# Kernel tuning notes

Measured on AMD Instinct MI355X. Metric: run time of the kernel, lower is better.

## Reference

```python
import jax, jax.numpy as jnp
import numpy as np

N_QUBITS = 2
N_PARAMS = 3 * N_QUBITS - 1  # = 5
B = 65536
C64 = jnp.complex64


def bkron(A, Bm):
    # batched Kronecker product: A [b,m,n], Bm [b,p,q] -> [b,m*p,n*q]
    b, m, n = A.shape
    _, p, q = Bm.shape
    return jnp.einsum('bij,bkl->bikjl', A, Bm).reshape(b, m * p, n * q)


def rx(theta):
    # exp(-0.5j*theta*X) = cos(t/2) I - i sin(t/2) X ; theta [b] real -> [b,2,2] complex
    c = jnp.cos(theta / 2).astype(C64)
    s = (-1j * jnp.sin(theta / 2)).astype(C64)
    return jnp.stack([jnp.stack([c, s], -1), jnp.stack([s, c], -1)], -2)


def ry(theta):
    # exp(-0.5j*theta*Y) = [[cos,-sin],[sin,cos]]
    c = jnp.cos(theta / 2).astype(C64)
    s = jnp.sin(theta / 2).astype(C64)
    return jnp.stack([jnp.stack([c, -s], -1), jnp.stack([s, c], -1)], -2)


def crx(theta):
    # kron(I2, |0><0|) + kron(Rx(theta), |1><1|)  (control on second qubit, as in source)
    b = theta.shape[0]
    P0 = jnp.array([[1, 0], [0, 0]], C64)
    P1 = jnp.array([[0, 0], [0, 1]], C64)
    I2 = jnp.eye(2, dtype=C64)
    term0 = jnp.kron(I2, P0)  # [4,4]
    term1 = bkron(rx(theta), jnp.broadcast_to(P1, (b, 2, 2)))
    return term0[None] + term1


def quantum_state(p):
    # p [b, >=5]; faithful to source: col 0 unused, Rx(p1) applied on both qubits
    first = bkron(rx(p[:, 1]), rx(p[:, 1]))          # recursiveRx, counter=1 base case
    second = bkron(ry(p[:, 2]), ry(p[:, 3]))         # recursiveRy, counter=3 base case
    rot = first @ second
    return rot @ crx(p[:, 4])                        # single CRx layer (N_Qubits=2)


def mlp(h, W1, b1, W2, b2, W3, b3, W4, b4):
    h = jax.nn.relu(h @ W1.T + b1)
    h = jax.nn.relu(h @ W2.T + b2)
    h = jax.nn.relu(h @ W3.T + b3)
    return h @ W4.T + b4


def mH(M):
    return jnp.conj(jnp.swapaxes(M, -1, -2))


def setup_inputs() -> dict:
    key = jax.random.key(0)
    ks = jax.random.split(key, 9)
    dims = [(200, 300), (100, 200), (50, 100), (N_PARAMS * 2, 50)]
    inp = {'x': jax.random.normal(ks[0], (B, 600), dtype=jnp.float32)}
    for i, (o, ii) in enumerate(dims):
        inp[f'W{i+1}'] = jax.random.normal(ks[1 + 2 * i], (o, ii), dtype=jnp.float32) * (1.0 / np.sqrt(ii))
        inp[f'b{i+1}'] = jax.random.normal(ks[2 + 2 * i], (o,), dtype=jnp.float32) * 0.01
    return inp


def reference(x, W1, b1, W2, b2, W3, b3, W4, b4):
    l1 = mlp(x[:, 0:300], W1, b1, W2, b2, W3, b3, W4, b4)   # [B, 10]
    l2 = mlp(x[:, 300:600], W1, b1, W2, b2, W3, b3, W4, b4)  # [B, 10]
    ket = jnp.zeros((4, 1), C64).at[0, 0].set(1.0)
    bra = jnp.zeros((1, 4), C64).at[0, 0].set(1.0)
    U2a = quantum_state(l2[:, :N_PARAMS])
    U2b = quantum_state(l2[:, N_PARAMS:])
    U1a = quantum_state(l1[:, :N_PARAMS])
    U1b = quantum_state(l1[:, N_PARAMS:])
    circuit1 = (bra[None] @ mH(U2a)) @ mH(U2b)   # [B,1,4]
    circuit2 = U1b @ (U1a @ ket[None])           # [B,4,1]
    inner = (circuit1 @ circuit2)[:, 0, 0]       # [B]
    fidelity = jnp.square(jnp.abs(inner))        # [B] real
    return fidelity
```

## Files before the change

kernel.cpp:

```cpp
#include <hip/hip_runtime.h>
#include <hip/hip_bf16.h>
#include <stdint.h>

typedef unsigned short u16;
typedef unsigned int   u32;
typedef __bf16 bf16x8 __attribute__((ext_vector_type(8)));
typedef float  f32x16 __attribute__((ext_vector_type(16)));

__device__ __forceinline__ u16 b2u(__bf16 b){ union U{__bf16 b; u16 u;} v; v.b=b; return v.u; }

__device__ __forceinline__ f32x16 MFMA(bf16x8 a, bf16x8 b, f32x16 c) {
  return __builtin_amdgcn_mfma_f32_32x32x16_bf16(a, b, c, 0, 0, 0);
}

#define OFF_WA  32768
#define OFF_WB  75776
#define LDS_BYTES 118784

constexpr int CH1 = 43008;
constexpr int CH2 = 32768;
constexpr int CH3 = 16384;
constexpr int CH4 = 8192;
constexpr long B1 = 0;
constexpr long B2 = 147L * 2048;
constexpr long B3 = 211L * 2048;
constexpr long B4 = 227L * 2048;

__global__ __launch_bounds__(64) void prep_kernel(
    const float* __restrict__ W1, const float* __restrict__ W2,
    const float* __restrict__ W3, const float* __restrict__ W4,
    u16* __restrict__ wf)
{
  int b = blockIdx.x, lane = threadIdx.x;
  const float* W; int NT, rel, Nv, Kv;
  if (b < 147)      { W = W1; NT = 7; rel = b;       Nv = 200; Kv = 300; }
  else if (b < 211) { W = W2; NT = 4; rel = b - 147; Nv = 100; Kv = 200; }
  else if (b < 227) { W = W3; NT = 2; rel = b - 211; Nv = 50;  Kv = 100; }
  else              { W = W4; NT = 1; rel = b - 227; Nv = 10;  Kv = 50;  }
  int kc = rel / NT, nt = rel % NT;
  int n  = nt*32 + (lane & 31);
  int kb = kc*16 + ((lane >> 5) << 3);
  u16* dst = wf + (size_t)b * 1024;
  #pragma unroll
  for (int j = 0; j < 8; ++j) {
    int k = kb + j;
    float w = (n < Nv && k < Kv) ? W[n*Kv + k] : 0.0f;
    __bf16 h = (__bf16)w;
    __bf16 l = (__bf16)(w - (float)h);
    dst[lane*8 + j]       = b2u(h);
    dst[512 + lane*8 + j] = b2u(l);
  }
}

template<int CHUNK>
__device__ __forceinline__ void stage_load(const char* __restrict__ g, float4* r, int tid) {
  constexpr int NS = (CHUNK + 8191) / 8192;
  #pragma unroll
  for (int it = 0; it < NS; ++it) {
    const int off = tid*16 + it*8192;
    if ((it+1)*8192 <= CHUNK)  r[it] = *(const float4*)(g + off);
    else if (off < CHUNK)      r[it] = *(const float4*)(g + off);
  }
}
template<int CHUNK>
__device__ __forceinline__ void stage_write(char* lds, const float4* r, int tid) {
  constexpr int NS = (CHUNK + 8191) / 8192;
  #pragma unroll
  for (int it = 0; it < NS; ++it) {
    const int off = tid*16 + it*8192;
    if ((it+1)*8192 <= CHUNK)  *(float4*)(lds + off) = r[it];
    else if (off < CHUNK)      *(float4*)(lds + off) = r[it];
  }
}
#define VMCNT0 asm volatile("s_waitcnt vmcnt(0)" ::: "memory")

template<int NTILES>
__device__ __forceinline__ void transition(
    const f32x16* acc, const float* __restrict__ bias, int nvalid,
    bf16x8* hh, bf16x8* hl, char* ms, int lane)
{
  #pragma unroll
  for (int j = 0; j < NTILES; ++j) {
    const int col = j*32 + (lane & 31);
    const float bv = (col < nvalid) ? bias[col] : 0.0f;
    #pragma unroll
    for (int r = 0; r < 16; ++r) {
      const int row = (r & 3) + ((r >> 2) << 3) + (((lane >> 5) & 1) << 2);
      float v = fmaxf(acc[j][r] + bv, 0.0f);
      __bf16 h = (__bf16)v;
      __bf16 l = (__bf16)(v - (float)h);
      const int bo = row*64 + (((lane & 31) << 1) ^ ((row & 3) << 4));
      *(u16*)(ms + bo)        = b2u(h);
      *(u16*)(ms + 2048 + bo) = b2u(l);
    }
    #pragma unroll
    for (int h2 = 0; h2 < 2; ++h2) {
      const int row = lane & 31;
      const int bo = row*64 + ((h2*32 + ((lane >> 5) << 4)) ^ ((row & 3) << 4));
      hh[2*j + h2] = *(const bf16x8*)(ms + bo);
      hl[2*j + h2] = *(const bf16x8*)(ms + 2048 + bo);
    }
  }
}

struct cpx { float r, i; };
__device__ __forceinline__ void ry_pair(float c, float s, cpx& a, cpx& b) {
  cpx na = { c*a.r - s*b.r, c*a.i - s*b.i };
  cpx nb = { s*a.r + c*b.r, s*a.i + c*b.i };
  a = na; b = nb;
}
__device__ __forceinline__ void rx_pair(float c, float s, cpx& a, cpx& b) {
  cpx na = { c*a.r + s*b.i, c*a.i - s*b.r };
  cpx nb = { s*a.i + c*b.r, -s*a.r + c*b.i };
  a = na; b = nb;
}
__device__ void build_state(const float* p, cpx v[4]) {
  float a1 = 0.5f*p[1], a2 = 0.5f*p[2], a3 = 0.5f*p[3];
  float c2 = cosf(a2), s2 = sinf(a2), c3 = cosf(a3), s3 = sinf(a3);
  v[0] = { c2*c3, 0.f }; v[1] = { c2*s3, 0.f };
  v[2] = { s2*c3, 0.f }; v[3] = { s2*s3, 0.f };
  float c1 = cosf(a1), s1 = sinf(a1);
  rx_pair(c1, s1, v[0], v[1]); rx_pair(c1, s1, v[2], v[3]);
  rx_pair(c1, s1, v[0], v[2]); rx_pair(c1, s1, v[1], v[3]);
  float q1 = 0.5f*p[6], q2 = 0.5f*p[7], q3 = 0.5f*p[8], q4 = 0.5f*p[9];
  float c4 = cosf(q4), s4 = sinf(q4);
  rx_pair(c4, s4, v[1], v[3]);
  float cc = cosf(q3), ss = sinf(q3);
  ry_pair(cc, ss, v[0], v[1]); ry_pair(cc, ss, v[2], v[3]);
  cc = cosf(q2); ss = sinf(q2);
  ry_pair(cc, ss, v[0], v[2]); ry_pair(cc, ss, v[1], v[3]);
  cc = cosf(q1); ss = sinf(q1);
  rx_pair(cc, ss, v[0], v[1]); rx_pair(cc, ss, v[2], v[3]);
  rx_pair(cc, ss, v[0], v[2]); rx_pair(cc, ss, v[1], v[3]);
}

__global__ __launch_bounds__(512, 2) void fused_kernel(
    const float* __restrict__ X,
    const float* __restrict__ b1p, const float* __restrict__ b2p,
    const float* __restrict__ b3p, const float* __restrict__ b4p,
    const u16* __restrict__ wf,
    float* __restrict__ out)
{
  __shared__ char lds[LDS_BYTES] __attribute__((aligned(16)));
  const int tid  = threadIdx.x;
  const int lane = tid & 63;
  const int wid  = tid >> 6;
  const long rowbase = (long)blockIdx.x*256 + wid*32;
  char* ms = lds + wid*4096;
  const char* wfc = (const char*)wf;

  float4 s0[6];
  stage_load<CH1>(wfc + B1, s0, tid);

  bf16x8 xf[19];
  {
    const float* xp = X + (rowbase + (lane & 31))*300 + ((lane >> 5) << 3);
    #pragma unroll
    for (int kc = 0; kc < 19; ++kc) {
      float4 f0 = *(const float4*)(xp + kc*16);
      float4 f1;
      if (kc == 18) {
        if (lane >= 32) f1 = make_float4(0.f, 0.f, 0.f, 0.f);
        else            f1 = *(const float4*)(xp + kc*16 + 4);
      } else {
        f1 = *(const float4*)(xp + kc*16 + 4);
      }
      xf[kc][0]=(__bf16)f0.x; xf[kc][1]=(__bf16)f0.y; xf[kc][2]=(__bf16)f0.z; xf[kc][3]=(__bf16)f0.w;
      xf[kc][4]=(__bf16)f1.x; xf[kc][5]=(__bf16)f1.y; xf[kc][6]=(__bf16)f1.z; xf[kc][7]=(__bf16)f1.w;
    }
  }
  VMCNT0;
  stage_write<CH1>(lds + OFF_WA, s0, tid);
  __syncthreads();

  f32x16 acc1[7] = {};
  #pragma unroll
  for (int step = 0; step < 7; ++step) {
    float4 sr[6];
    if (step < 6) stage_load<CH1>(wfc + B1 + (size_t)(step+1)*CH1, sr, tid);
    const char* wb = lds + ((step & 1) ? OFF_WB : OFF_WA);
    #pragma unroll
    for (int kk = 0; kk < 3; ++kk) {
      const int kc = step*3 + kk;
      if (kc < 19) {
        const bf16x8 ah = xf[kc];
        #pragma unroll
        for (int nt = 0; nt < 7; ++nt) {
          const char* bp = wb + (kk*7 + nt)*2048 + lane*16;
          bf16x8 bh = *(const bf16x8*)bp;
          bf16x8 bl = *(const bf16x8*)(bp + 1024);
          acc1[nt] = MFMA(ah, bh, acc1[nt]);
          acc1[nt] = MFMA(ah, bl, acc1[nt]);
        }
      }
    }
    if (step < 6) { VMCNT0; stage_write<CH1>(lds + ((step & 1) ? OFF_WA : OFF_WB), sr, tid); }
    __syncthreads();
  }

  float4 s2[4];
  stage_load<CH2>(wfc + B2, s2, tid);
  bf16x8 h1h[14], h1l[14];
  transition<7>(acc1, b1p, 200, h1h, h1l, ms, lane);
  VMCNT0;
  stage_write<CH2>(lds + OFF_WA, s2, tid);
  __syncthreads();

  f32x16 acc2[4] = {};
  #pragma unroll
  for (int step = 0; step < 4; ++step) {
    float4 sr[4];
    if (step < 3) stage_load<CH2>(wfc + B2 + (size_t)(step+1)*CH2, sr, tid);
    const char* wb = lds + ((step & 1) ? OFF_WB : OFF_WA);
    #pragma unroll
    for (int kk = 0; kk < 4; ++kk) {
      const int kc = step*4 + kk;
      if (kc < 14) {
        #pragma unroll
        for (int nt = 0; nt < 4; ++nt) {
          const char* bp = wb + (kk*4 + nt)*2048 + lane*16;
          bf16x8 bh = *(const bf16x8*)bp;
          bf16x8 bl = *(const bf16x8*)(bp + 1024);
          acc2[nt] = MFMA(h1h[kc], bh, acc2[nt]);
          acc2[nt] = MFMA(h1h[kc], bl, acc2[nt]);
          acc2[nt] = MFMA(h1l[kc], bh, acc2[nt]);
        }
      }
    }
    if (step < 3) { VMCNT0; stage_write<CH2>(lds + ((step & 1) ? OFF_WA : OFF_WB), sr, tid); }
    __syncthreads();
  }

  float4 s3[2];
  stage_load<CH3>(wfc + B3, s3, tid);
  bf16x8 h2h[8], h2l[8];
  transition<4>(acc2, b2p, 100, h2h, h2l, ms, lane);
  VMCNT0;
  stage_write<CH3>(lds + OFF_WA, s3, tid);
  __syncthreads();

  f32x16 acc3[2] = {};
  #pragma unroll
  for (int step = 0; step < 2; ++step) {
    float4 sr[2];
    if (step < 1) stage_load<CH3>(wfc + B3 + (size_t)CH3, sr, tid);
    const char* wb = lds + ((step & 1) ? OFF_WB : OFF_WA);
    #pragma unroll
    for (int kk = 0; kk < 4; ++kk) {
      const int kc = step*4 + kk;
      #pragma unroll
      for (int nt = 0; nt < 2; ++nt) {
        const char* bp = wb + (kk*2 + nt)*2048 + lane*16;
        bf16x8 bh = *(const bf16x8*)bp;
        bf16x8 bl = *(const bf16x8*)(bp + 1024);
        acc3[nt] = MFMA(h2h[kc], bh, acc3[nt]);
        acc3[nt] = MFMA(h2h[kc], bl, acc3[nt]);
        acc3[nt] = MFMA(h2l[kc], bh, acc3[nt]);
      }
    }
    if (step < 1) { VMCNT0; stage_write<CH3>(lds + OFF_WB, sr, tid); }
    __syncthreads();
  }

  float4 s4[1];
  stage_load<CH4>(wfc + B4, s4, tid);
  bf16x8 h3h[4], h3l[4];
  transition<2>(acc3, b3p, 50, h3h, h3l, ms, lane);
  VMCNT0;
  stage_write<CH4>(lds + OFF_WA, s4, tid);
  __syncthreads();

  f32x16 acc4 = {};
  {
    const char* wb = lds + OFF_WA;
    #pragma unroll
    for (int kk = 0; kk < 4; ++kk) {
      const char* bp = wb + kk*2048 + lane*16;
      bf16x8 bh = *(const bf16x8*)bp;
      bf16x8 bl = *(const bf16x8*)(bp + 1024);
      acc4 = MFMA(h3h[kk], bh, acc4);
      acc4 = MFMA(h3h[kk], bl, acc4);
      acc4 = MFMA(h3l[kk], bh, acc4);
    }
  }

  {
    float* sp = (float*)ms;
    #pragma unroll
    for (int r = 0; r < 16; ++r) {
      const int row = (r & 3) + ((r >> 2) << 3) + (((lane >> 5) & 1) << 2);
      const int col = lane & 31;
      sp[row*32 + col] = acc4[r] + ((col < 10) ? b4p[col] : 0.0f);
    }
    if (lane < 16) {
      float p1[10], p2[10];
      #pragma unroll
      for (int j = 0; j < 10; ++j) {
        p1[j] = sp[(2*lane)*32 + j];
        p2[j] = sp[(2*lane + 1)*32 + j];
      }
      cpx v[4], w[4];
      build_state(p1, v);
      build_state(p2, w);
      float ir = 0.f, ii = 0.f;
      #pragma unroll
      for (int k = 0; k < 4; ++k) {
        ir += w[k].r*v[k].r + w[k].i*v[k].i;
        ii += w[k].r*v[k].i - w[k].i*v[k].r;
      }
      out[(size_t)blockIdx.x*128 + wid*16 + lane] = ir*ir + ii*ii;
    }
  }
}

extern "C" void kernel_launch(void* const* d_in, const int* in_sizes, int n_in,
                              void* d_out, int out_size, void* d_ws, size_t ws_size,
                              hipStream_t stream)
{
  const float* X  = (const float*)d_in[0];
  const float* W1 = (const float*)d_in[1];
  const float* b1 = (const float*)d_in[2];
  const float* W2 = (const float*)d_in[3];
  const float* b2 = (const float*)d_in[4];
  const float* W3 = (const float*)d_in[5];
  const float* b3 = (const float*)d_in[6];
  const float* W4 = (const float*)d_in[7];
  const float* b4 = (const float*)d_in[8];
  u16* wf = (u16*)d_ws;

  prep_kernel<<<dim3(231), dim3(64), 0, stream>>>(W1, W2, W3, W4, wf);
  fused_kernel<<<dim3(512), dim3(512), 0, stream>>>(X, b1, b2, b3, b4, wf, (float*)d_out);
}
```

Measured before the change: 356.2 us.

## Switch fused MLP to 16x16x32 MFMA tiles with smaller LDS footprint

Replaces the 32x32x16 MFMA path with 16x16x32 bf16 MFMA. Each wave now handles 16 rows instead of 32, and the grid doubles to 1024 blocks. The weight fragment layout in prep is redone to match, LDS use drops so four blocks can be resident per CU, and X is streamed per k-chunk rather than held entirely in registers. The goal is higher occupancy and lower register pressure. The cost is that weights are reloaded from LDS twice as often per row and there are more sync steps.

```diff
diff --git a/kernel.cpp b/kernel.cpp
--- a/kernel.cpp
+++ b/kernel.cpp
@@ -4,27 +4,28 @@
 
 typedef unsigned short u16;
 typedef unsigned int   u32;
+typedef unsigned long long u64;
 typedef __bf16 bf16x8 __attribute__((ext_vector_type(8)));
-typedef float  f32x16 __attribute__((ext_vector_type(16)));
+typedef float  f32x4  __attribute__((ext_vector_type(4)));
 
 __device__ __forceinline__ u16 b2u(__bf16 b){ union U{__bf16 b; u16 u;} v; v.b=b; return v.u; }
 
-__device__ __forceinline__ f32x16 MFMA(bf16x8 a, bf16x8 b, f32x16 c) {
-  return __builtin_amdgcn_mfma_f32_32x32x16_bf16(a, b, c, 0, 0, 0);
-}
-
-#define OFF_WA  32768
-#define OFF_WB  75776
-#define LDS_BYTES 118784
-
-constexpr int CH1 = 43008;
-constexpr int CH2 = 32768;
-constexpr int CH3 = 16384;
-constexpr int CH4 = 8192;
-constexpr long B1 = 0;
-constexpr long B2 = 147L * 2048;
-constexpr long B3 = 211L * 2048;
-constexpr long B4 = 227L * 2048;
+__device__ __forceinline__ f32x4 MFMA16(bf16x8 a, bf16x8 b, f32x4 c) {
+  return __builtin_amdgcn_mfma_f32_16x16x32_bf16(a, b, c, 0, 0, 0);
+}
+
+#define LDS_WA   0
+#define LDS_WB   14336
+#define LDS_SCR  28672
+#define SCR_STRIDE 2304
+#define LDS_TOTAL 47104
+
+#define BL2 140
+#define BL3 189
+#define BL4 205
+#define NBLOCKS 207
+
+#define VMCNT0 asm volatile("s_waitcnt vmcnt(0)" ::: "memory")
 
 __global__ __launch_bounds__(64) void prep_kernel(
     const float* __restrict__ W1, const float* __restrict__ W2,
@@ -33,22 +34,22 @@
 {
   int b = blockIdx.x, lane = threadIdx.x;
   const float* W; int NT, rel, Nv, Kv;
-  if (b < 147)      { W = W1; NT = 7; rel = b;       Nv = 200; Kv = 300; }
-  else if (b < 211) { W = W2; NT = 4; rel = b - 147; Nv = 100; Kv = 200; }
-  else if (b < 227) { W = W3; NT = 2; rel = b - 211; Nv = 50;  Kv = 100; }
-  else              { W = W4; NT = 1; rel = b - 227; Nv = 10;  Kv = 50;  }
+  if (b < BL2)      { W = W1; NT = 14; rel = b;       Nv = 200; Kv = 300; }
+  else if (b < BL3) { W = W2; NT = 7;  rel = b - BL2; Nv = 100; Kv = 200; }
+  else if (b < BL4) { W = W3; NT = 4;  rel = b - BL3; Nv = 50;  Kv = 100; }
+  else              { W = W4; NT = 1;  rel = b - BL4; Nv = 10;  Kv = 50;  }
   int kc = rel / NT, nt = rel % NT;
-  int n  = nt*32 + (lane & 31);
-  int kb = kc*16 + ((lane >> 5) << 3);
+  int n  = nt * 16 + (lane & 15);
+  int kb = kc * 32 + ((lane >> 4) << 3);
   u16* dst = wf + (size_t)b * 1024;
   #pragma unroll
   for (int j = 0; j < 8; ++j) {
     int k = kb + j;
-    float w = (n < Nv && k < Kv) ? W[n*Kv + k] : 0.0f;
+    float w = (n < Nv && k < Kv) ? W[n * Kv + k] : 0.0f;
     __bf16 h = (__bf16)w;
     __bf16 l = (__bf16)(w - (float)h);
-    dst[lane*8 + j]       = b2u(h);
-    dst[512 + lane*8 + j] = b2u(l);
+    dst[lane * 8 + j]       = b2u(h);
+    dst[512 + lane * 8 + j] = b2u(l);
   }
 }
 
@@ -57,9 +58,9 @@
   constexpr int NS = (CHUNK + 8191) / 8192;
   #pragma unroll
   for (int it = 0; it < NS; ++it) {
-    const int off = tid*16 + it*8192;
-    if ((it+1)*8192 <= CHUNK)  r[it] = *(const float4*)(g + off);
-    else if (off < CHUNK)      r[it] = *(const float4*)(g + off);
+    const int off = tid * 16 + it * 8192;
+    if ((it + 1) * 8192 <= CHUNK) r[it] = *(const float4*)(g + off);
+    else if (off < CHUNK)         r[it] = *(const float4*)(g + off);
   }
 }
 template<int CHUNK>
@@ -67,39 +68,75 @@
   constexpr int NS = (CHUNK + 8191) / 8192;
   #pragma unroll
   for (int it = 0; it < NS; ++it) {
-    const int off = tid*16 + it*8192;
-    if ((it+1)*8192 <= CHUNK)  *(float4*)(lds + off) = r[it];
-    else if (off < CHUNK)      *(float4*)(lds + off) = r[it];
-  }
-}
-#define VMCNT0 asm volatile("s_waitcnt vmcnt(0)" ::: "memory")
-
-template<int NTILES>
-__device__ __forceinline__ void transition(
-    const f32x16* acc, const float* __restrict__ bias, int nvalid,
-    bf16x8* hh, bf16x8* hl, char* ms, int lane)
-{
-  #pragma unroll
-  for (int j = 0; j < NTILES; ++j) {
-    const int col = j*32 + (lane & 31);
-    const float bv = (col < nvalid) ? bias[col] : 0.0f;
+    const int off = tid * 16 + it * 8192;
+    if ((it + 1) * 8192 <= CHUNK) *(float4*)(lds + off) = r[it];
+    else if (off < CHUNK)         *(float4*)(lds + off) = r[it];
+  }
+}
+
+template<int TIN>
+__device__ __forceinline__ void transition(const f32x4* acc,
+    const float* __restrict__ bias, int nvalid,
+    bf16x8* oh, bf16x8* ol, char* scr, int lane)
+{
+  const int col = lane & 15, q = lane >> 4;
+  float bv[TIN];
+  #pragma unroll
+  for (int t = 0; t < TIN; ++t) {
+    const int n = t * 16 + col;
+    bv[t] = (n < nvalid) ? bias[n] : 0.0f;
+  }
+  constexpr int KC = (TIN + 1) / 2;
+  #pragma unroll
+  for (int kc = 0; kc < KC; ++kc) {
     #pragma unroll
-    for (int r = 0; r < 16; ++r) {
-      const int row = (r & 3) + ((r >> 2) << 3) + (((lane >> 5) & 1) << 2);
-      float v = fmaxf(acc[j][r] + bv, 0.0f);
-      __bf16 h = (__bf16)v;
-      __bf16 l = (__bf16)(v - (float)h);
-      const int bo = row*64 + (((lane & 31) << 1) ^ ((row & 3) << 4));
-      *(u16*)(ms + bo)        = b2u(h);
-      *(u16*)(ms + 2048 + bo) = b2u(l);
-    }
+    for (int hh = 0; hh < 2; ++hh) {
+      const int t = 2 * kc + hh;
+      #pragma unroll
+      for (int r = 0; r < 4; ++r) {
+        float v = 0.0f;
+        if (t < TIN) v = fmaxf(acc[t][r] + bv[t], 0.0f);
+        __bf16 h = (__bf16)v;
+        __bf16 l = (__bf16)(v - (float)h);
+        const int m = q * 4 + r;
+        char* wp = scr + m * 72 + (hh * 16 + col) * 2;
+        *(u16*)wp           = b2u(h);
+        *(u16*)(wp + 1152)  = b2u(l);
+      }
+    }
+    asm volatile("s_waitcnt lgkmcnt(0)" ::: "memory");
+    const char* rp = scr + col * 72 + q * 16;
+    union { u64 u[2]; bf16x8 v; } ph, pl;
+    ph.u[0] = *(const u64*)(rp);
+    ph.u[1] = *(const u64*)(rp + 8);
+    pl.u[0] = *(const u64*)(rp + 1152);
+    pl.u[1] = *(const u64*)(rp + 1160);
+    oh[kc] = ph.v;
+    ol[kc] = pl.v;
+  }
+}
+
+template<int NT, int NKC>
+__device__ __forceinline__ void layerN(char* lds, const char* wl,
+    f32x4* acc, const bf16x8* ah, const bf16x8* al, int lane, int tid)
+{
+  constexpr int CH = NT * 2048;
+  #pragma unroll
+  for (int s = 0; s < NKC; ++s) {
+    float4 sr[(CH + 8191) / 8192];
+    if (s + 1 < NKC) stage_load<CH>(wl + (size_t)(s + 1) * CH, sr, tid);
+    const char* wb = lds + ((s & 1) ? LDS_WB : LDS_WA);
     #pragma unroll
-    for (int h2 = 0; h2 < 2; ++h2) {
-      const int row = lane & 31;
-      const int bo = row*64 + ((h2*32 + ((lane >> 5) << 4)) ^ ((row & 3) << 4));
-      hh[2*j + h2] = *(const bf16x8*)(ms + bo);
-      hl[2*j + h2] = *(const bf16x8*)(ms + 2048 + bo);
-    }
+    for (int nt = 0; nt < NT; ++nt) {
+      const char* bp = wb + nt * 2048 + (size_t)lane * 16;
+      bf16x8 bh = *(const bf16x8*)bp;
+      bf16x8 bl = *(const bf16x8*)(bp + 1024);
+      acc[nt] = MFMA16(ah[s], bh, acc[nt]);
+      acc[nt] = MFMA16(ah[s], bl, acc[nt]);
+      acc[nt] = MFMA16(al[s], bh, acc[nt]);
+    }
+    if (s + 1 < NKC) { VMCNT0; stage_write<CH>(lds + ((s & 1) ? LDS_WA : LDS_WB), sr, tid); }
+    __syncthreads();
   }
 }
 
@@ -134,170 +171,114 @@
   rx_pair(cc, ss, v[0], v[2]); rx_pair(cc, ss, v[1], v[3]);
 }
 
-__global__ __launch_bounds__(512, 2) void fused_kernel(
+__device__ __forceinline__ bf16x8 cvt8(float4 a, float4 b) {
+  bf16x8 r;
+  r[0]=(__bf16)a.x; r[1]=(__bf16)a.y; r[2]=(__bf16)a.z; r[3]=(__bf16)a.w;
+  r[4]=(__bf16)b.x; r[5]=(__bf16)b.y; r[6]=(__bf16)b.z; r[7]=(__bf16)b.w;
+  return r;
+}
+__device__ __forceinline__ void loadX(const float* xp, int kc, int q,
+                                      float4& a, float4& b) {
+  int k0 = kc * 32 + q * 8;
+  a = (k0     < 300) ? *(const float4*)(xp + k0)     : make_float4(0,0,0,0);
+  b = (k0 + 4 < 300) ? *(const float4*)(xp + k0 + 4) : make_float4(0,0,0,0);
+}
+
+__global__ __launch_bounds__(512, 4) void fused_kernel(
     const float* __restrict__ X,
     const float* __restrict__ b1p, const float* __restrict__ b2p,
     const float* __restrict__ b3p, const float* __restrict__ b4p,
     const u16* __restrict__ wf,
     float* __restrict__ out)
 {
-  __shared__ char lds[LDS_BYTES] __attribute__((aligned(16)));
+  __shared__ char lds[LDS_TOTAL] __attribute__((aligned(16)));
   const int tid  = threadIdx.x;
   const int lane = tid & 63;
   const int wid  = tid >> 6;
-  const long rowbase = (long)blockIdx.x*256 + wid*32;
-  char* ms = lds + wid*4096;
+  const int q    = lane >> 4;
+  char* scr = lds + LDS_SCR + wid * SCR_STRIDE;
   const char* wfc = (const char*)wf;
-
-  float4 s0[6];
-  stage_load<CH1>(wfc + B1, s0, tid);
-
-  bf16x8 xf[19];
-  {
-    const float* xp = X + (rowbase + (lane & 31))*300 + ((lane >> 5) << 3);
+  const long rowbase = (long)blockIdx.x * 128 + wid * 16;
+  const float* xp = X + (rowbase + (lane & 15)) * 300;
+
+  float4 s0[2];
+  stage_load<14336>(wfc, s0, tid);
+  float4 fxa, fxb;
+  loadX(xp, 0, q, fxa, fxb);
+  VMCNT0;
+  stage_write<14336>(lds + LDS_WA, s0, tid);
+  bf16x8 xcur = cvt8(fxa, fxb);
+  __syncthreads();
+
+  f32x4 acc1[14] = {};
+  #pragma unroll
+  for (int s = 0; s < 20; ++s) {
+    float4 sr[2];
+    if (s < 19) stage_load<14336>(wfc + (size_t)(s + 1) * 14336, sr, tid);
+    if (!(s & 1) && s < 18) loadX(xp, (s >> 1) + 1, q, fxa, fxb);
+    const char* wb = lds + ((s & 1) ? LDS_WB : LDS_WA);
+    f32x4* acch = acc1 + (s & 1) * 7;
     #pragma unroll
-    for (int kc = 0; kc < 19; ++kc) {
-      float4 f0 = *(const float4*)(xp + kc*16);
-      float4 f1;
-      if (kc == 18) {
-        if (lane >= 32) f1 = make_float4(0.f, 0.f, 0.f, 0.f);
-        else            f1 = *(const float4*)(xp + kc*16 + 4);
-      } else {
-        f1 = *(const float4*)(xp + kc*16 + 4);
-      }
-      xf[kc][0]=(__bf16)f0.x; xf[kc][1]=(__bf16)f0.y; xf[kc][2]=(__bf16)f0.z; xf[kc][3]=(__bf16)f0.w;
-      xf[kc][4]=(__bf16)f1.x; xf[kc][5]=(__bf16)f1.y; xf[kc][6]=(__bf16)f1.z; xf[kc][7]=(__bf16)f1.w;
-    }
-  }
-  VMCNT0;
-  stage_write<CH1>(lds + OFF_WA, s0, tid);
-  __syncthreads();
-
-  f32x16 acc1[7] = {};
-  #pragma unroll
-  for (int step = 0; step < 7; ++step) {
-    float4 sr[6];
-    if (step < 6) stage_load<CH1>(wfc + B1 + (size_t)(step+1)*CH1, sr, tid);
-    const char* wb = lds + ((step & 1) ? OFF_WB : OFF_WA);
-    #pragma unroll
-    for (int kk = 0; kk < 3; ++kk) {
-      const int kc = step*3 + kk;
-      if (kc < 19) {
-        const bf16x8 ah = xf[kc];
-        #pragma unroll
-        for (int nt = 0; nt < 7; ++nt) {
-          const char* bp = wb + (kk*7 + nt)*2048 + lane*16;
-          bf16x8 bh = *(const bf16x8*)bp;
-          bf16x8 bl = *(const bf16x8*)(bp + 1024);
-          acc1[nt] = MFMA(ah, bh, acc1[nt]);
-          acc1[nt] = MFMA(ah, bl, acc1[nt]);
-        }
-      }
-    }
-    if (step < 6) { VMCNT0; stage_write<CH1>(lds + ((step & 1) ? OFF_WA : OFF_WB), sr, tid); }
-    __syncthreads();
-  }
-
-  float4 s2[4];
-  stage_load<CH2>(wfc + B2, s2, tid);
-  bf16x8 h1h[14], h1l[14];
-  transition<7>(acc1, b1p, 200, h1h, h1l, ms, lane);
-  VMCNT0;
-  stage_write<CH2>(lds + OFF_WA, s2, tid);
-  __syncthreads();
-
-  f32x16 acc2[4] = {};
-  #pragma unroll
-  for (int step = 0; step < 4; ++step) {
-    float4 sr[4];
-    if (step < 3) stage_load<CH2>(wfc + B2 + (size_t)(step+1)*CH2, sr, tid);
-    const char* wb = lds + ((step & 1) ? OFF_WB : OFF_WA);
-    #pragma unroll
-    for (int kk = 0; kk < 4; ++kk) {
-      const int kc = step*4 + kk;
-      if (kc < 14) {
-        #pragma unroll
-        for (int nt = 0; nt < 4; ++nt) {
-          const char* bp = wb + (kk*4 + nt)*2048 + lane*16;
-          bf16x8 bh = *(const bf16x8*)bp;
-          bf16x8 bl = *(const bf16x8*)(bp + 1024);
-          acc2[nt] = MFMA(h1h[kc], bh, acc2[nt]);
-          acc2[nt] = MFMA(h1h[kc], bl, acc2[nt]);
-          acc2[nt] = MFMA(h1l[kc], bh, acc2[nt]);
-        }
-      }
-    }
-    if (step < 3) { VMCNT0; stage_write<CH2>(lds + ((step & 1) ? OFF_WA : OFF_WB), sr, tid); }
-    __syncthreads();
-  }
-
-  float4 s3[2];
-  stage_load<CH3>(wfc + B3, s3, tid);
-  bf16x8 h2h[8], h2l[8];
-  transition<4>(acc2, b2p, 100, h2h, h2l, ms, lane);
-  VMCNT0;
-  stage_write<CH3>(lds + OFF_WA, s3, tid);
-  __syncthreads();
-
-  f32x16 acc3[2] = {};
-  #pragma unroll
-  for (int step = 0; step < 2; ++step) {
-    float4 sr[2];
-    if (step < 1) stage_load<CH3>(wfc + B3 + (size_t)CH3, sr, tid);
-    const char* wb = lds + ((step & 1) ? OFF_WB : OFF_WA);
-    #pragma unroll
-    for (int kk = 0; kk < 4; ++kk) {
-      const int kc = step*4 + kk;
-      #pragma unroll
-      for (int nt = 0; nt < 2; ++nt) {
-        const char* bp = wb + (kk*2 + nt)*2048 + lane*16;
-        bf16x8 bh = *(const bf16x8*)bp;
-        bf16x8 bl = *(const bf16x8*)(bp + 1024);
-        acc3[nt] = MFMA(h2h[kc], bh, acc3[nt]);
-        acc3[nt] = MFMA(h2h[kc], bl, acc3[nt]);
-        acc3[nt] = MFMA(h2l[kc], bh, acc3[nt]);
-      }
-    }
-    if (step < 1) { VMCNT0; stage_write<CH3>(lds + OFF_WB, sr, tid); }
-    __syncthreads();
-  }
-
-  float4 s4[1];
-  stage_load<CH4>(wfc + B4, s4, tid);
-  bf16x8 h3h[4], h3l[4];
-  transition<2>(acc3, b3p, 50, h3h, h3l, ms, lane);
-  VMCNT0;
-  stage_write<CH4>(lds + OFF_WA, s4, tid);
-  __syncthreads();
-
-  f32x16 acc4 = {};
-  {
-    const char* wb = lds + OFF_WA;
-    #pragma unroll
-    for (int kk = 0; kk < 4; ++kk) {
-      const char* bp = wb + kk*2048 + lane*16;
+    for (int nt = 0; nt < 7; ++nt) {
+      const char* bp = wb + nt * 2048 + (size_t)lane * 16;
       bf16x8 bh = *(const bf16x8*)bp;
       bf16x8 bl = *(const bf16x8*)(bp + 1024);
-      acc4 = MFMA(h3h[kk], bh, acc4);
-      acc4 = MFMA(h3h[kk], bl, acc4);
-      acc4 = MFMA(h3l[kk], bh, acc4);
-    }
-  }
+      acch[nt] = MFMA16(xcur, bh, acch[nt]);
+      acch[nt] = MFMA16(xcur, bl, acch[nt]);
+    }
+    if (s < 19) { VMCNT0; stage_write<14336>(lds + ((s & 1) ? LDS_WA : LDS_WB), sr, tid); }
+    if ((s & 1) && s < 19) xcur = cvt8(fxa, fxb);
+    __syncthreads();
+  }
+
+  float4 s2[2];
+  stage_load<14336>(wfc + (size_t)BL2 * 2048, s2, tid);
+  bf16x8 h1h[7], h1l[7];
+  transition<14>(acc1, b1p, 200, h1h, h1l, scr, lane);
+  VMCNT0;
+  stage_write<14336>(lds + LDS_WA, s2, tid);
+  __syncthreads();
+
+  f32x4 acc2[7] = {};
+  layerN<7, 7>(lds, wfc + (size_t)BL2 * 2048, acc2, h1h, h1l, lane, tid);
+
+  float4 s3[1];
+  stage_load<8192>(wfc + (size_t)BL3 * 2048, s3, tid);
+  bf16x8 h2h[4], h2l[4];
+  transition<7>(acc2, b2p, 100, h2h, h2l, scr, lane);
+  VMCNT0;
+  stage_write<8192>(lds + LDS_WA, s3, tid);
+  __syncthreads();
+
+  f32x4 acc3[4] = {};
+  layerN<4, 4>(lds, wfc + (size_t)BL3 * 2048, acc3, h2h, h2l, lane, tid);
+
+  float4 s4[1];
+  stage_load<2048>(wfc + (size_t)BL4 * 2048, s4, tid);
+  bf16x8 h3h[2], h3l[2];
+  transition<4>(acc3, b3p, 50, h3h, h3l, scr, lane);
+  VMCNT0;
+  stage_write<2048>(lds + LDS_WA, s4, tid);
+  __syncthreads();
+
+  f32x4 acc4[1] = {};
+  layerN<1, 2>(lds, wfc + (size_t)BL4 * 2048, acc4, h3h, h3l, lane, tid);
 
   {
-    float* sp = (float*)ms;
+    const int col = lane & 15;
+    float* sp = (float*)scr;
     #pragma unroll
-    for (int r = 0; r < 16; ++r) {
-      const int row = (r & 3) + ((r >> 2) << 3) + (((lane >> 5) & 1) << 2);
-      const int col = lane & 31;
-      sp[row*32 + col] = acc4[r] + ((col < 10) ? b4p[col] : 0.0f);
-    }
-    if (lane < 16) {
+    for (int r = 0; r < 4; ++r) {
+      const int row = q * 4 + r;
+      sp[row * 16 + col] = acc4[0][r] + ((col < 10) ? b4p[col] : 0.0f);
+    }
+    asm volatile("s_waitcnt lgkmcnt(0)" ::: "memory");
+    if (lane < 8) {
       float p1[10], p2[10];
       #pragma unroll
       for (int j = 0; j < 10; ++j) {
-        p1[j] = sp[(2*lane)*32 + j];
-        p2[j] = sp[(2*lane + 1)*32 + j];
+        p1[j] = sp[(2 * lane) * 16 + j];
+        p2[j] = sp[(2 * lane + 1) * 16 + j];
       }
       cpx v[4], w[4];
       build_state(p1, v);
@@ -308,7 +289,7 @@
         ir += w[k].r*v[k].r + w[k].i*v[k].i;
         ii += w[k].r*v[k].i - w[k].i*v[k].r;
       }
-      out[(size_t)blockIdx.x*128 + wid*16 + lane] = ir*ir + ii*ii;
+      out[(size_t)blockIdx.x * 64 + wid * 8 + lane] = ir*ir + ii*ii;
     }
   }
 }
@@ -328,6 +309,7 @@
   const float* b4 = (const float*)d_in[8];
   u16* wf = (u16*)d_ws;
 
-  prep_kernel<<<dim3(231), dim3(64), 0, stream>>>(W1, W2, W3, W4, wf);
-  fused_kernel<<<dim3(512), dim3(512), 0, stream>>>(X, b1, b2, b3, b4, wf, (float*)d_out);
-}
+  prep_kernel<<<dim3(NBLOCKS), dim3(64), 0, stream>>>(W1, W2, W3, W4, wf);
+  fused_kernel<<<dim3(1024), dim3(512), 0, stream>>>(X, b1, b2, b3, b4, wf,
+                                                     (float*)d_out);
+}
```

After: 370.5 us. +4.0%, slower.
